# Kernel tuning notes

Hardware: AMD Instinct MI355X
Metric: run time of the kernel (lower is better)

## Reference

```python
import jax, jax.numpy as jnp
import numpy as np

WS = 12      # window_size
OV = 6       # overlap
STEP = WS - OV
EPS = 1e-5   # LayerNorm eps (torch default)


def setup_inputs() -> dict:
    key = jax.random.key(0)
    ks = jax.random.split(key, 6)
    B, L, H, Dh = 4, 4092, 8, 64
    d_model = H * Dh
    sc = 1.0 / np.sqrt(Dh)
    return {
        "queries": jax.random.normal(ks[0], (B, L, H, Dh), dtype=jnp.float32),
        "keys": jax.random.normal(ks[1], (B, L, H, Dh), dtype=jnp.float32),
        "values": jax.random.normal(ks[2], (B, L, H, Dh), dtype=jnp.float32),
        "Wq": jax.random.normal(ks[3], (Dh, Dh), dtype=jnp.float32) * sc,
        "Wk": jax.random.normal(ks[4], (Dh, Dh), dtype=jnp.float32) * sc,
        "Wv": jax.random.normal(ks[5], (Dh, Dh), dtype=jnp.float32) * sc,
        "gamma": jnp.ones((d_model,), dtype=jnp.float32),
        "beta": jnp.zeros((d_model,), dtype=jnp.float32),
    }


def reference(queries, keys, values, Wq, Wk, Wv, gamma, beta):
    # input layout: [B, L, H, Dh]
    B, L, H, Dh = queries.shape
    nw = (L - OV) // STEP                       # number of windows
    Lc = WS + STEP * (nw - 1)                   # reconstructed length (== L)
    idx = jnp.arange(nw)[:, None] * STEP + jnp.arange(WS)[None, :]  # [nw, WS]

    def windows(x):
        # [B,L,H,Dh] -> [B,H,nw,WS,Dh]
        return jnp.transpose(x, (0, 2, 1, 3))[:, :, idx, :]

    qw, kw, vw = windows(queries), windows(keys), windows(values)
    # per-head-dim linear projections (nn.Linear: x @ W.T)
    Q = jnp.einsum('bhnwd,ed->bhnwe', qw, Wq)
    K = jnp.einsum('bhnwd,ed->bhnwe', kw, Wk)
    V = jnp.einsum('bhnwd,ed->bhnwe', vw, Wv)

    scores = jnp.einsum('bhnqd,bhnkd->bhnqk', Q, K) / jnp.sqrt(jnp.asarray(Dh, Q.dtype))
    attn = jax.nn.softmax(scores, axis=-1)      # [B,H,nw,WS,WS]
    ow = jnp.einsum('bhnqk,bhnkd->bhnqd', attn, V)

    # [B,H,nw,WS,Dh] -> [B,nw,WS,H*Dh]
    attn_out = jnp.transpose(ow, (0, 2, 3, 1, 4)).reshape(B, nw, WS, H * Dh)

    # overlap-add + averaging
    flat_idx = idx.reshape(-1)                  # [nw*WS]
    acc = jnp.zeros((B, Lc, H * Dh), dtype=attn_out.dtype)
    acc = acc.at[:, flat_idx, :].add(attn_out.reshape(B, nw * WS, H * Dh))
    cnt = jnp.zeros((Lc,), dtype=attn_out.dtype).at[flat_idx].add(1.0)
    out = acc / cnt[None, :, None]

    # residual + LayerNorm
    resid = queries.reshape(B, L, H * Dh)
    x = out + resid
    mu = jnp.mean(x, axis=-1, keepdims=True)
    var = jnp.mean((x - mu) ** 2, axis=-1, keepdims=True)
    z = (x - mu) / jnp.sqrt(var + EPS) * gamma + beta
    return z, attn
```

## Files before the change

### kernel.cpp

```cpp
#include <hip/hip_runtime.h>
#include <math.h>

#define B_    4
#define L_    4092
#define H_    8
#define DH    64
#define DM    512
#define WS_   12
#define STEP_ 6
#define NW    681
#define NC    682
#define EPS_  1e-5f
#define Z_ELEMS (B_*L_*DM)

typedef __attribute__((ext_vector_type(8))) short short8;
typedef __attribute__((ext_vector_type(4))) float floatx4;
typedef unsigned short u16;

__device__ __forceinline__ u16 f2bf(float f) {
    union { float f; unsigned u; } x; x.f = f;
    unsigned u = x.u;
    return (u16)((u + 0x7FFFu + ((u >> 16) & 1u)) >> 16);
}
__device__ __forceinline__ short8 pack8(float4 a, float4 b) {
    short8 r;
    r[0] = (short)f2bf(a.x); r[1] = (short)f2bf(a.y);
    r[2] = (short)f2bf(a.z); r[3] = (short)f2bf(a.w);
    r[4] = (short)f2bf(b.x); r[5] = (short)f2bf(b.y);
    r[6] = (short)f2bf(b.z); r[7] = (short)f2bf(b.w);
    return r;
}

__global__ __launch_bounds__(256) void proj_kernel(
    const float* __restrict__ q, const float* __restrict__ k, const float* __restrict__ v,
    const float* __restrict__ Wq, const float* __restrict__ Wk, const float* __restrict__ Wv,
    u16* __restrict__ Qp, u16* __restrict__ Kp, u16* __restrict__ Vp)
{
    const int tensor = blockIdx.y;
    const float* __restrict__ X = (tensor == 0) ? q  : (tensor == 1) ? k  : v;
    const float* __restrict__ W = (tensor == 0) ? Wq : (tensor == 1) ? Wk : Wv;
    u16* __restrict__ Y         = (tensor == 0) ? Qp : (tensor == 1) ? Kp : Vp;

    const int t = threadIdx.x, lane = t & 63, wv = t >> 6;
    const int m = lane & 15, q3 = lane >> 4;

    short8 wf[4][2];
    #pragma unroll
    for (int nt = 0; nt < 4; ++nt)
        #pragma unroll
        for (int kc = 0; kc < 2; ++kc) {
            const float* wp = W + (nt * 16 + m) * 64 + kc * 32 + q3 * 8;
            wf[nt][kc] = pack8(*(const float4*)wp, *(const float4*)(wp + 4));
        }

    const int waveId = blockIdx.x * 4 + wv;
    for (int tile = waveId; tile < 8184; tile += 2048) {
        const int rbase = tile * 16;
        const int r = rbase + m;
        const int bh = r / L_;
        const int l = r - bh * L_;
        const int b = bh >> 3, h = bh & 7;
        const float* xp = X + (((size_t)b * L_ + l) * H_ + h) * 64;
        short8 a0 = pack8(*(const float4*)(xp + q3 * 8),      *(const float4*)(xp + q3 * 8 + 4));
        short8 a1 = pack8(*(const float4*)(xp + 32 + q3 * 8), *(const float4*)(xp + 32 + q3 * 8 + 4));

        floatx4 acc[4];
        #pragma unroll
        for (int nt = 0; nt < 4; ++nt) {
            floatx4 c = {0.f, 0.f, 0.f, 0.f};
            c = __builtin_amdgcn_mfma_f32_16x16x32_bf16(a0, wf[nt][0], c, 0, 0, 0);
            c = __builtin_amdgcn_mfma_f32_16x16x32_bf16(a1, wf[nt][1], c, 0, 0, 0);
            acc[nt] = c;
        }
        #pragma unroll
        for (int reg = 0; reg < 4; ++reg) {
            const size_t rowoff = (size_t)(rbase + q3 * 4 + reg) * 64;
            #pragma unroll
            for (int nt = 0; nt < 4; ++nt)
                Y[rowoff + nt * 16 + m] = f2bf(acc[nt][reg]);
        }
    }
}

__device__ __forceinline__ void window_attn(
    const u16* __restrict__ Qb, const u16* __restrict__ Kb, const u16* __restrict__ Vb,
    float* __restrict__ attn_out , float* __restrict__ Pl,
    int w, int lane, floatx4 o[4])
{
    const int m = lane & 15, q3 = lane >> 4;
    const size_t rb = (size_t)(w * 6 + m) * 64;

    short8 aq0 = *(const short8*)(Qb + rb + q3 * 8);
    short8 aq1 = *(const short8*)(Qb + rb + 32 + q3 * 8);
    short8 bk0 = *(const short8*)(Kb + rb + q3 * 8);
    short8 bk1 = *(const short8*)(Kb + rb + 32 + q3 * 8);

    floatx4 s4 = {0.f, 0.f, 0.f, 0.f};
    s4 = __builtin_amdgcn_mfma_f32_16x16x32_bf16(aq0, bk0, s4, 0, 0, 0);
    s4 = __builtin_amdgcn_mfma_f32_16x16x32_bf16(aq1, bk1, s4, 0, 0, 0);

    float p[4];
    #pragma unroll
    for (int r = 0; r < 4; ++r) {
        float s = (m < 12) ? s4[r] * 0.125f : -1e30f;
        float mx = s;
        #pragma unroll
        for (int off = 1; off < 16; off <<= 1)
            mx = fmaxf(mx, __shfl_xor(mx, off, 16));
        float e = __expf(s - mx);
        float sum = e;
        #pragma unroll
        for (int off = 1; off < 16; off <<= 1)
            sum += __shfl_xor(sum, off, 16);
        p[r] = e / sum;
    }

    if (attn_out && m < 12 && q3 < 3) {
        #pragma unroll
        for (int r = 0; r < 4; ++r)
            attn_out[(q3 * 4 + r) * 12 + m] = p[r];
    }

    #pragma unroll
    for (int r = 0; r < 4; ++r)
        Pl[(q3 * 4 + r) * 20 + m] = p[r];
    short8 ap = {0, 0, 0, 0, 0, 0, 0, 0};
    if (q3 < 2) {
        float4 f0 = *(const float4*)&Pl[m * 20 + q3 * 8];
        float4 f1 = *(const float4*)&Pl[m * 20 + q3 * 8 + 4];
        ap = pack8(f0, f1);
    }

    const int w6 = w * 6;
    #pragma unroll
    for (int nt = 0; nt < 4; ++nt) {
        short8 bv;
        #pragma unroll
        for (int jj = 0; jj < 8; ++jj)
            bv[jj] = (short)Vb[(size_t)(w6 + q3 * 8 + jj) * 64 + nt * 16 + m];
        floatx4 oo = {0.f, 0.f, 0.f, 0.f};
        oo = __builtin_amdgcn_mfma_f32_16x16x32_bf16(ap, bv, oo, 0, 0, 0);
        o[nt] = oo;
    }
}

__global__ __launch_bounds__(256) void attn_kernel(
    const u16* __restrict__ Qp, const u16* __restrict__ Kp, const u16* __restrict__ Vp,
    float* __restrict__ attn, float* __restrict__ z)
{
    __shared__ float P_lds[4][16 * 20];
    __shared__ float Oacc[4][6 * 64];
    const int t = threadIdx.x, lane = t & 63, wv = t >> 6;
    const int m = lane & 15, q3 = lane >> 4;
    const int c = blockIdx.x * 4 + wv;
    const int h = blockIdx.y, b = blockIdx.z;
    if (c >= NC) return;
    const int bh = b * H_ + h;
    const u16* Qb = Qp + (size_t)bh * L_ * 64;
    const u16* Kb = Kp + (size_t)bh * L_ * 64;
    const u16* Vb = Vp + (size_t)bh * L_ * 64;
    float* Pl = P_lds[wv];
    float* Oa = Oacc[wv];
    const bool hasA = (c < NW), hasB = (c > 0);
    const float scale = (hasA && hasB) ? 0.5f : 1.0f;

    floatx4 oA[4], oB[4];
    if (hasA) {
        float* ao = attn + ((size_t)bh * NW + c) * (WS_ * WS_);
        window_attn(Qb, Kb, Vb, ao, Pl, c, lane, oA);
        if (hasB) {
            #pragma unroll
            for (int r = 0; r < 4; ++r) {
                const int row = q3 * 4 + r;
                if (row < 6) {
                    #pragma unroll
                    for (int nt = 0; nt < 4; ++nt)
                        Oa[row * 64 + nt * 16 + m] = oA[nt][r];
                }
            }
        } else {
            #pragma unroll
            for (int r = 0; r < 4; ++r) {
                const int row = q3 * 4 + r;
                if (row < 6) {
                    #pragma unroll
                    for (int nt = 0; nt < 4; ++nt)
                        z[((size_t)b * L_ + row) * DM + h * 64 + nt * 16 + m] = oA[nt][r];
                }
            }
        }
    }
    if (hasB) {
        window_attn(Qb, Kb, Vb, nullptr, Pl, c - 1, lane, oB);
        #pragma unroll
        for (int r = 0; r < 4; ++r) {
            const int row = q3 * 4 + r;
            if (row >= 6 && row < 12) {
                const int rr = row - 6;
                #pragma unroll
                for (int nt = 0; nt < 4; ++nt) {
                    float val = oB[nt][r];
                    if (hasA) val += Oa[rr * 64 + nt * 16 + m];
                    z[((size_t)b * L_ + c * 6 + rr) * DM + h * 64 + nt * 16 + m] = val * scale;
                }
            }
        }
    }
}

__global__ __launch_bounds__(256) void ln_kernel(
    const float* __restrict__ qres, const float* __restrict__ gamma,
    const float* __restrict__ beta, float* __restrict__ z)
{
    const int t = threadIdx.x;
    const int rr = t >> 7;
    const int tt = t & 127;
    const size_t row = (size_t)blockIdx.x * 2 + rr;
    const int c = tt * 4;

    float4 a  = *(const float4*)(z + row * DM + c);
    float4 r4 = *(const float4*)(qres + row * DM + c);
    float4 x = make_float4(a.x + r4.x, a.y + r4.y, a.z + r4.z, a.w + r4.w);

    float s1 = x.x + x.y + x.z + x.w;
    float s2 = x.x * x.x + x.y * x.y + x.z * x.z + x.w * x.w;
    #pragma unroll
    for (int off = 1; off < 64; off <<= 1) {
        s1 += __shfl_xor(s1, off, 64);
        s2 += __shfl_xor(s2, off, 64);
    }
    __shared__ float red[4][2];
    const int wid = t >> 6;
    if ((t & 63) == 0) { red[wid][0] = s1; red[wid][1] = s2; }
    __syncthreads();
    const int wp = wid & 2;
    s1 = red[wp][0] + red[wp + 1][0];
    s2 = red[wp][1] + red[wp + 1][1];
    const float mu  = s1 * (1.0f / 512.0f);
    const float var = s2 * (1.0f / 512.0f) - mu * mu;
    const float inv = 1.0f / sqrtf(var + EPS_);

    float4 g4 = *(const float4*)(gamma + c);
    float4 b4 = *(const float4*)(beta + c);
    float4 o;
    o.x = (x.x - mu) * inv * g4.x + b4.x;
    o.y = (x.y - mu) * inv * g4.y + b4.y;
    o.z = (x.z - mu) * inv * g4.z + b4.z;
    o.w = (x.w - mu) * inv * g4.w + b4.w;
    *(float4*)(z + row * DM + c) = o;
}

extern "C" void kernel_launch(void* const* d_in, const int* in_sizes, int n_in,
                              void* d_out, int out_size, void* d_ws, size_t ws_size,
                              hipStream_t stream) {
    const float* q     = (const float*)d_in[0];
    const float* k     = (const float*)d_in[1];
    const float* v     = (const float*)d_in[2];
    const float* Wq    = (const float*)d_in[3];
    const float* Wk    = (const float*)d_in[4];
    const float* Wv    = (const float*)d_in[5];
    const float* gamma = (const float*)d_in[6];
    const float* beta  = (const float*)d_in[7];

    float* z    = (float*)d_out;
    float* attn = (float*)d_out + Z_ELEMS;

    u16* Qp = (u16*)d_ws;
    u16* Kp = Qp + (size_t)B_ * H_ * L_ * 64;
    u16* Vp = Kp + (size_t)B_ * H_ * L_ * 64;

    proj_kernel<<<dim3(512, 3, 1), 256, 0, stream>>>(q, k, v, Wq, Wk, Wv, Qp, Kp, Vp);
    attn_kernel<<<dim3((NC + 3) / 4, H_, B_), 256, 0, stream>>>(Qp, Kp, Vp, attn, z);
    ln_kernel<<<(B_ * L_) / 2, 256, 0, stream>>>(q, gamma, beta, z);
}
```

Measured before the change: 213.9 us.

## Fuse attention with LayerNorm per chunk and stage V in shared memory

Merges the attention and LayerNorm kernels into one kernel. Each block handles one 6-row chunk across all 8 heads, accumulates the overlap-add result in shared memory, then applies residual plus LayerNorm in place, so the fp32 intermediate z is never written and re-read from global memory. V rows for the chunk are staged into LDS with vector loads instead of strided scalar global gathers. The projection output is permuted so each lane can store four bf16 values at once. The cost is extra block-wide barriers and a reduced block count (682x4 blocks of 512 threads), which may lower occupancy.

```diff
diff --git a/kernel.cpp b/kernel.cpp
--- a/kernel.cpp
+++ b/kernel.cpp
@@ -49,7 +49,7 @@
     for (int nt = 0; nt < 4; ++nt)
         #pragma unroll
         for (int kc = 0; kc < 2; ++kc) {
-            const float* wp = W + (nt * 16 + m) * 64 + kc * 32 + q3 * 8;
+            const float* wp = W + (4 * m + nt) * 64 + kc * 32 + q3 * 8;
             wf[nt][kc] = pack8(*(const float4*)wp, *(const float4*)(wp + 4));
         }
 
@@ -74,18 +74,19 @@
         }
         #pragma unroll
         for (int reg = 0; reg < 4; ++reg) {
-            const size_t rowoff = (size_t)(rbase + q3 * 4 + reg) * 64;
-            #pragma unroll
-            for (int nt = 0; nt < 4; ++nt)
-                Y[rowoff + nt * 16 + m] = f2bf(acc[nt][reg]);
+            const int row = rbase + q3 * 4 + reg;
+            ushort4 o4;
+            o4.x = f2bf(acc[0][reg]); o4.y = f2bf(acc[1][reg]);
+            o4.z = f2bf(acc[2][reg]); o4.w = f2bf(acc[3][reg]);
+            *(ushort4*)(Y + (size_t)row * 64 + 4 * m) = o4;
         }
     }
 }
 
 __device__ __forceinline__ void window_attn(
-    const u16* __restrict__ Qb, const u16* __restrict__ Kb, const u16* __restrict__ Vb,
-    float* __restrict__ attn_out , float* __restrict__ Pl,
-    int w, int lane, floatx4 o[4])
+    const u16* __restrict__ Qb, const u16* __restrict__ Kb, const u16* __restrict__ VsH,
+    float* __restrict__ attn_out , float* __restrict__ PlF,
+    int w, int off, int lane, floatx4 o[4])
 {
     const int m = lane & 15, q3 = lane >> 4;
     const size_t rb = (size_t)(w * 6 + m) * 64;
@@ -105,13 +106,13 @@
         float s = (m < 12) ? s4[r] * 0.125f : -1e30f;
         float mx = s;
         #pragma unroll
-        for (int off = 1; off < 16; off <<= 1)
-            mx = fmaxf(mx, __shfl_xor(mx, off, 16));
+        for (int o2 = 1; o2 < 16; o2 <<= 1)
+            mx = fmaxf(mx, __shfl_xor(mx, o2, 16));
         float e = __expf(s - mx);
         float sum = e;
         #pragma unroll
-        for (int off = 1; off < 16; off <<= 1)
-            sum += __shfl_xor(sum, off, 16);
+        for (int o2 = 1; o2 < 16; o2 <<= 1)
+            sum += __shfl_xor(sum, o2, 16);
         p[r] = e / sum;
     }
 
@@ -123,75 +124,85 @@
 
     #pragma unroll
     for (int r = 0; r < 4; ++r)
-        Pl[(q3 * 4 + r) * 20 + m] = p[r];
+        PlF[(q3 * 4 + r) * 20 + m] = p[r];
+    __syncthreads();
     short8 ap = {0, 0, 0, 0, 0, 0, 0, 0};
     if (q3 < 2) {
-        float4 f0 = *(const float4*)&Pl[m * 20 + q3 * 8];
-        float4 f1 = *(const float4*)&Pl[m * 20 + q3 * 8 + 4];
+        float4 f0 = *(const float4*)&PlF[m * 20 + q3 * 8];
+        float4 f1 = *(const float4*)&PlF[m * 20 + q3 * 8 + 4];
         ap = pack8(f0, f1);
     }
 
-    const int w6 = w * 6;
     #pragma unroll
     for (int nt = 0; nt < 4; ++nt) {
-        short8 bv;
-        #pragma unroll
-        for (int jj = 0; jj < 8; ++jj)
-            bv[jj] = (short)Vb[(size_t)(w6 + q3 * 8 + jj) * 64 + nt * 16 + m];
+        short8 bv = {0, 0, 0, 0, 0, 0, 0, 0};
+        if (q3 == 0) {
+            #pragma unroll
+            for (int jj = 0; jj < 8; ++jj)
+                bv[jj] = (short)VsH[(off + jj) * 64 + nt * 16 + m];
+        } else if (q3 == 1) {
+            #pragma unroll
+            for (int jj = 0; jj < 4; ++jj)
+                bv[jj] = (short)VsH[(off + 8 + jj) * 64 + nt * 16 + m];
+        }
         floatx4 oo = {0.f, 0.f, 0.f, 0.f};
         oo = __builtin_amdgcn_mfma_f32_16x16x32_bf16(ap, bv, oo, 0, 0, 0);
         o[nt] = oo;
     }
 }
 
-__global__ __launch_bounds__(256) void attn_kernel(
+__global__ __launch_bounds__(512) void attn_ln_kernel(
     const u16* __restrict__ Qp, const u16* __restrict__ Kp, const u16* __restrict__ Vp,
-    float* __restrict__ attn, float* __restrict__ z)
+    const float* __restrict__ qres, const float* __restrict__ gamma,
+    const float* __restrict__ beta, float* __restrict__ attn, float* __restrict__ z)
 {
-    __shared__ float P_lds[4][16 * 20];
-    __shared__ float Oacc[4][6 * 64];
-    const int t = threadIdx.x, lane = t & 63, wv = t >> 6;
+    __shared__ alignas(16) u16   Vs[8][18][64];
+    __shared__ alignas(16) float Pl[8][16 * 20];
+    __shared__ alignas(16) float Xs[6][512];
+
+    const int c = blockIdx.x, b = blockIdx.y;
+    const int t = threadIdx.x, lane = t & 63, h = t >> 6;
     const int m = lane & 15, q3 = lane >> 4;
-    const int c = blockIdx.x * 4 + wv;
-    const int h = blockIdx.y, b = blockIdx.z;
-    if (c >= NC) return;
-    const int bh = b * H_ + h;
+
+    const int lbase = c * 6 - 6;
+    for (int i = t; i < 2304; i += 512) {
+        const int hh  = i / 288;
+        const int rem = i - hh * 288;
+        const int rr  = rem >> 4;
+        const int cc  = (rem & 15) * 4;
+        const int l = lbase + rr;
+        if (l >= 0 && l < L_)
+            *(ushort4*)&Vs[hh][rr][cc] =
+                *(const ushort4*)(Vp + ((size_t)(b * 8 + hh) * L_ + l) * 64 + cc);
+    }
+    __syncthreads();
+
+    const int bh = b * 8 + h;
     const u16* Qb = Qp + (size_t)bh * L_ * 64;
     const u16* Kb = Kp + (size_t)bh * L_ * 64;
-    const u16* Vb = Vp + (size_t)bh * L_ * 64;
-    float* Pl = P_lds[wv];
-    float* Oa = Oacc[wv];
+    const u16* VsH = &Vs[h][0][0];
+    float* PlH = &Pl[h][0];
+
     const bool hasA = (c < NW), hasB = (c > 0);
     const float scale = (hasA && hasB) ? 0.5f : 1.0f;
 
     floatx4 oA[4], oB[4];
     if (hasA) {
         float* ao = attn + ((size_t)bh * NW + c) * (WS_ * WS_);
-        window_attn(Qb, Kb, Vb, ao, Pl, c, lane, oA);
-        if (hasB) {
-            #pragma unroll
-            for (int r = 0; r < 4; ++r) {
-                const int row = q3 * 4 + r;
-                if (row < 6) {
-                    #pragma unroll
-                    for (int nt = 0; nt < 4; ++nt)
-                        Oa[row * 64 + nt * 16 + m] = oA[nt][r];
-                }
+        window_attn(Qb, Kb, VsH, ao, PlH, c, 6, lane, oA);
+        #pragma unroll
+        for (int r = 0; r < 4; ++r) {
+            const int row = q3 * 4 + r;
+            if (row < 6) {
+                #pragma unroll
+                for (int nt = 0; nt < 4; ++nt)
+                    Xs[row][h * 64 + nt * 16 + m] = oA[nt][r];
             }
-        } else {
-            #pragma unroll
-            for (int r = 0; r < 4; ++r) {
-                const int row = q3 * 4 + r;
-                if (row < 6) {
-                    #pragma unroll
-                    for (int nt = 0; nt < 4; ++nt)
-                        z[((size_t)b * L_ + row) * DM + h * 64 + nt * 16 + m] = oA[nt][r];
-                }
-            }
-        }
-    }
+        }
+    }
+    __syncthreads();
     if (hasB) {
-        window_attn(Qb, Kb, Vb, nullptr, Pl, c - 1, lane, oB);
+        window_attn(Qb, Kb, VsH, nullptr, PlH, c - 1, 0, lane, oB);
         #pragma unroll
         for (int r = 0; r < 4; ++r) {
             const int row = q3 * 4 + r;
@@ -200,54 +211,54 @@
                 #pragma unroll
                 for (int nt = 0; nt < 4; ++nt) {
                     float val = oB[nt][r];
-                    if (hasA) val += Oa[rr * 64 + nt * 16 + m];
-                    z[((size_t)b * L_ + c * 6 + rr) * DM + h * 64 + nt * 16 + m] = val * scale;
+                    if (hasA) val += Xs[rr][h * 64 + nt * 16 + m];
+                    Xs[rr][h * 64 + nt * 16 + m] = val * scale;
                 }
             }
         }
     }
-}
-
-__global__ __launch_bounds__(256) void ln_kernel(
-    const float* __restrict__ qres, const float* __restrict__ gamma,
-    const float* __restrict__ beta, float* __restrict__ z)
-{
-    const int t = threadIdx.x;
-    const int rr = t >> 7;
-    const int tt = t & 127;
-    const size_t row = (size_t)blockIdx.x * 2 + rr;
-    const int c = tt * 4;
-
-    float4 a  = *(const float4*)(z + row * DM + c);
-    float4 r4 = *(const float4*)(qres + row * DM + c);
-    float4 x = make_float4(a.x + r4.x, a.y + r4.y, a.z + r4.z, a.w + r4.w);
-
-    float s1 = x.x + x.y + x.z + x.w;
-    float s2 = x.x * x.x + x.y * x.y + x.z * x.z + x.w * x.w;
-    #pragma unroll
-    for (int off = 1; off < 64; off <<= 1) {
-        s1 += __shfl_xor(s1, off, 64);
-        s2 += __shfl_xor(s2, off, 64);
-    }
-    __shared__ float red[4][2];
-    const int wid = t >> 6;
-    if ((t & 63) == 0) { red[wid][0] = s1; red[wid][1] = s2; }
-    __syncthreads();
-    const int wp = wid & 2;
-    s1 = red[wp][0] + red[wp + 1][0];
-    s2 = red[wp][1] + red[wp + 1][1];
-    const float mu  = s1 * (1.0f / 512.0f);
-    const float var = s2 * (1.0f / 512.0f) - mu * mu;
-    const float inv = 1.0f / sqrtf(var + EPS_);
-
-    float4 g4 = *(const float4*)(gamma + c);
-    float4 b4 = *(const float4*)(beta + c);
-    float4 o;
-    o.x = (x.x - mu) * inv * g4.x + b4.x;
-    o.y = (x.y - mu) * inv * g4.y + b4.y;
-    o.z = (x.z - mu) * inv * g4.z + b4.z;
-    o.w = (x.w - mu) * inv * g4.w + b4.w;
-    *(float4*)(z + row * DM + c) = o;
+    __syncthreads();
+
+    if (h < 6) {
+        const int l = c * 6 + h;
+        const int cc = lane * 8;
+        float4 xa = *(const float4*)&Xs[h][cc];
+        float4 xb = *(const float4*)&Xs[h][cc + 4];
+        const float* qr = qres + ((size_t)b * L_ + l) * DM + cc;
+        const float4 ra = *(const float4*)qr;
+        const float4 rb2 = *(const float4*)(qr + 4);
+        xa.x += ra.x;  xa.y += ra.y;  xa.z += ra.z;  xa.w += ra.w;
+        xb.x += rb2.x; xb.y += rb2.y; xb.z += rb2.z; xb.w += rb2.w;
+
+        float s1 = xa.x + xa.y + xa.z + xa.w + xb.x + xb.y + xb.z + xb.w;
+        float s2 = xa.x*xa.x + xa.y*xa.y + xa.z*xa.z + xa.w*xa.w
+                 + xb.x*xb.x + xb.y*xb.y + xb.z*xb.z + xb.w*xb.w;
+        #pragma unroll
+        for (int off = 1; off < 64; off <<= 1) {
+            s1 += __shfl_xor(s1, off, 64);
+            s2 += __shfl_xor(s2, off, 64);
+        }
+        const float mu  = s1 * (1.0f / 512.0f);
+        const float var = s2 * (1.0f / 512.0f) - mu * mu;
+        const float inv = 1.0f / sqrtf(var + EPS_);
+
+        const float4 ga = *(const float4*)(gamma + cc);
+        const float4 gb = *(const float4*)(gamma + cc + 4);
+        const float4 ba = *(const float4*)(beta + cc);
+        const float4 bb = *(const float4*)(beta + cc + 4);
+        float4 oa, ob;
+        oa.x = (xa.x - mu) * inv * ga.x + ba.x;
+        oa.y = (xa.y - mu) * inv * ga.y + ba.y;
+        oa.z = (xa.z - mu) * inv * ga.z + ba.z;
+        oa.w = (xa.w - mu) * inv * ga.w + ba.w;
+        ob.x = (xb.x - mu) * inv * gb.x + bb.x;
+        ob.y = (xb.y - mu) * inv * gb.y + bb.y;
+        ob.z = (xb.z - mu) * inv * gb.z + bb.z;
+        ob.w = (xb.w - mu) * inv * gb.w + bb.w;
+        float* zp = z + ((size_t)b * L_ + l) * DM + cc;
+        *(float4*)zp = oa;
+        *(float4*)(zp + 4) = ob;
+    }
 }
 
 extern "C" void kernel_launch(void* const* d_in, const int* in_sizes, int n_in,
@@ -270,6 +281,5 @@
     u16* Vp = Kp + (size_t)B_ * H_ * L_ * 64;
 
     proj_kernel<<<dim3(512, 3, 1), 256, 0, stream>>>(q, k, v, Wq, Wk, Wv, Qp, Kp, Vp);
-    attn_kernel<<<dim3((NC + 3) / 4, H_, B_), 256, 0, stream>>>(Qp, Kp, Vp, attn, z);
-    ln_kernel<<<(B_ * L_) / 2, 256, 0, stream>>>(q, gamma, beta, z);
-}
+    attn_ln_kernel<<<dim3(NC, B_), 512, 0, stream>>>(Qp, Kp, Vp, q, gamma, beta, attn, z);
+}
```

Result: faster. 203.3 us (-5.0%).
